# Kernel optimization log

Measured on AMD Instinct MI355X. Metric: run time of the kernel, lower is better.

## Reference

```python
import jax, jax.numpy as jnp
import numpy as np

T = 4096          # number of combine applications (segment length)
TRACE = 64        # trace_size (memory_size)
CTX = 64          # context_size


def setup_inputs() -> dict:
    key = jax.random.key(0)
    k1, k2, k3, k4 = jax.random.split(key, 4)
    shape = (T, TRACE, CTX)
    # deterministic FFM params (init_deterministic)
    a = jnp.linspace(1e-6, 0.5, TRACE).astype(jnp.float32)
    b = (2 * jnp.pi / jnp.linspace(1, 1000, CTX)).astype(jnp.float32)
    return {
        "a": a,
        "b": b,
        "state_re": jax.random.normal(k1, shape, jnp.float32),
        "state_im": jax.random.normal(k2, shape, jnp.float32),
        "x_re": jax.random.normal(k3, shape, jnp.float32),
        "x_im": jax.random.normal(k4, shape, jnp.float32),
        "i": jnp.ones((T,), jnp.int32),
        "j": jnp.ones((T,), jnp.int32),
    }


def reference(a, b, state_re, state_im, x_re, x_im, i, j):
    # log_gamma: (-|a| + i*b) * t, broadcast to [T, TRACE, CTX]
    t = j.astype(jnp.float32).reshape(-1, 1, 1)
    ab = jax.lax.complex(-jnp.abs(a).reshape(1, TRACE, 1),
                         b.reshape(1, 1, CTX))
    gamma = jnp.exp(ab * t)                       # complex decay/rotation gate
    state = jax.lax.complex(state_re, state_im)
    x = jax.lax.complex(x_re, x_im)
    new_state = state * gamma + x                 # binary associative combine
    return (jnp.real(new_state), jnp.imag(new_state), j + i)
```

## Files before the change

kernel.cpp:

```cpp
#include <hip/hip_runtime.h>


typedef float f32x4 __attribute__((ext_vector_type(4)));

constexpr int T_DIM  = 4096;
constexpr int N      = T_DIM * 64 * 64;
constexpr int N4     = N / 4;
constexpr int GRID   = 2048;
constexpr int BLOCK  = 256;
constexpr int STRIDE = GRID * BLOCK;
constexpr int TRIPS  = N4 / STRIDE;
constexpr int T_STEP = STRIDE >> 10;

__global__ __launch_bounds__(BLOCK, 8) void ffm_kernel(
    const float* __restrict__ a,
    const float* __restrict__ b,
    const float* __restrict__ s_re,
    const float* __restrict__ s_im,
    const float* __restrict__ x_re,
    const float* __restrict__ x_im,
    const int*   __restrict__ iv,
    const int*   __restrict__ jv,
    float* __restrict__ out)
{
    const int gtid = blockIdx.x * blockDim.x + threadIdx.x;

    if (gtid < T_DIM) {
        out[2 * N + gtid] = (float)(jv[gtid] + iv[gtid]);
    }

    const int c4 = (gtid & 15) << 2;
    const int m  = (gtid >> 4) & 63;
    const int t0 = gtid >> 10;

    const float am = fabsf(a[m]);
    const f32x4 bv = *reinterpret_cast<const f32x4*>(b + c4);

    int base = gtid << 2;

    f32x4 sr = *reinterpret_cast<const f32x4*>(s_re + base);
    f32x4 si = *reinterpret_cast<const f32x4*>(s_im + base);
    f32x4 xr = *reinterpret_cast<const f32x4*>(x_re + base);
    f32x4 xi = *reinterpret_cast<const f32x4*>(x_im + base);
    float tj = (float)jv[t0];

    #pragma unroll
    for (int trip = 0; trip < TRIPS; ++trip) {
        f32x4 nsr, nsi, nxr, nxi;
        float ntj = 0.f;
        const int nbase = base + (STRIDE << 2);
        if (trip + 1 < TRIPS) {
            nsr = *reinterpret_cast<const f32x4*>(s_re + nbase);
            nsi = *reinterpret_cast<const f32x4*>(s_im + nbase);
            nxr = *reinterpret_cast<const f32x4*>(x_re + nbase);
            nxi = *reinterpret_cast<const f32x4*>(x_im + nbase);
            ntj = (float)jv[t0 + (trip + 1) * T_STEP];
        }

        const float decay = __expf(-am * tj);
        f32x4 orv, oiv;
        #pragma unroll
        for (int k = 0; k < 4; ++k) {
            float s, c;
            __sincosf(bv[k] * tj, &s, &c);
            const float gre = decay * c;
            const float gim = decay * s;
            orv[k] = fmaf(sr[k], gre, fmaf(-si[k], gim, xr[k]));
            oiv[k] = fmaf(sr[k], gim, fmaf( si[k], gre, xi[k]));
        }

        *reinterpret_cast<f32x4*>(out + base)     = orv;
        *reinterpret_cast<f32x4*>(out + N + base) = oiv;

        if (trip + 1 < TRIPS) {
            sr = nsr; si = nsi; xr = nxr; xi = nxi; tj = ntj;
            base = nbase;
        }
    }
}

extern "C" void kernel_launch(void* const* d_in, const int* in_sizes, int n_in,
                              void* d_out, int out_size, void* d_ws, size_t ws_size,
                              hipStream_t stream) {
    const float* a    = (const float*)d_in[0];
    const float* b    = (const float*)d_in[1];
    const float* s_re = (const float*)d_in[2];
    const float* s_im = (const float*)d_in[3];
    const float* x_re = (const float*)d_in[4];
    const float* x_im = (const float*)d_in[5];
    const int*   iv   = (const int*)d_in[6];
    const int*   jv   = (const int*)d_in[7];
    float* out = (float*)d_out;

    ffm_kernel<<<GRID, BLOCK, 0, stream>>>(a, b, s_re, s_im, x_re, x_im, iv, jv, out);
}
```

Baseline: 81.10 us.

## Issue all loads up front per thread and double grid size

New measurement: 89.26 us. +10.1%, slower.

```diff
diff --git a/kernel.cpp b/kernel.cpp
--- a/kernel.cpp
+++ b/kernel.cpp
@@ -6,13 +6,12 @@
 constexpr int T_DIM  = 4096;
 constexpr int N      = T_DIM * 64 * 64;
 constexpr int N4     = N / 4;
-constexpr int GRID   = 2048;
+constexpr int GRID   = 4096;
 constexpr int BLOCK  = 256;
 constexpr int STRIDE = GRID * BLOCK;
-constexpr int TRIPS  = N4 / STRIDE;
-constexpr int T_STEP = STRIDE >> 10;
+constexpr int ITEMS  = N4 / STRIDE;
 
-__global__ __launch_bounds__(BLOCK, 8) void ffm_kernel(
+__global__ __launch_bounds__(BLOCK) void ffm_kernel(
     const float* __restrict__ a,
     const float* __restrict__ b,
     const float* __restrict__ s_re,
@@ -36,46 +35,40 @@
     const float am = fabsf(a[m]);
     const f32x4 bv = *reinterpret_cast<const f32x4*>(b + c4);
 
-    int base = gtid << 2;
+    float tj[ITEMS];
+    #pragma unroll
+    for (int i = 0; i < ITEMS; ++i) {
+        tj[i] = (float)jv[t0 + (i << 10)];
+    }
 
-    f32x4 sr = *reinterpret_cast<const f32x4*>(s_re + base);
-    f32x4 si = *reinterpret_cast<const f32x4*>(s_im + base);
-    f32x4 xr = *reinterpret_cast<const f32x4*>(x_re + base);
-    f32x4 xi = *reinterpret_cast<const f32x4*>(x_im + base);
-    float tj = (float)jv[t0];
+    f32x4 sr[ITEMS], si[ITEMS], xr[ITEMS], xi[ITEMS];
+    #pragma unroll
+    for (int i = 0; i < ITEMS; ++i) {
+        const int base = (gtid + i * STRIDE) << 2;
+        sr[i] = *reinterpret_cast<const f32x4*>(s_re + base);
+        si[i] = *reinterpret_cast<const f32x4*>(s_im + base);
+        xr[i] = *reinterpret_cast<const f32x4*>(x_re + base);
+        xi[i] = *reinterpret_cast<const f32x4*>(x_im + base);
+    }
+
+    __builtin_amdgcn_sched_barrier(0);
 
     #pragma unroll
-    for (int trip = 0; trip < TRIPS; ++trip) {
-        f32x4 nsr, nsi, nxr, nxi;
-        float ntj = 0.f;
-        const int nbase = base + (STRIDE << 2);
-        if (trip + 1 < TRIPS) {
-            nsr = *reinterpret_cast<const f32x4*>(s_re + nbase);
-            nsi = *reinterpret_cast<const f32x4*>(s_im + nbase);
-            nxr = *reinterpret_cast<const f32x4*>(x_re + nbase);
-            nxi = *reinterpret_cast<const f32x4*>(x_im + nbase);
-            ntj = (float)jv[t0 + (trip + 1) * T_STEP];
-        }
-
-        const float decay = __expf(-am * tj);
+    for (int i = 0; i < ITEMS; ++i) {
+        const float decay = __expf(-am * tj[i]);
         f32x4 orv, oiv;
         #pragma unroll
         for (int k = 0; k < 4; ++k) {
             float s, c;
-            __sincosf(bv[k] * tj, &s, &c);
+            __sincosf(bv[k] * tj[i], &s, &c);
             const float gre = decay * c;
             const float gim = decay * s;
-            orv[k] = fmaf(sr[k], gre, fmaf(-si[k], gim, xr[k]));
-            oiv[k] = fmaf(sr[k], gim, fmaf( si[k], gre, xi[k]));
+            orv[k] = fmaf(sr[i][k], gre, fmaf(-si[i][k], gim, xr[i][k]));
+            oiv[k] = fmaf(sr[i][k], gim, fmaf( si[i][k], gre, xi[i][k]));
         }
-
+        const int base = (gtid + i * STRIDE) << 2;
         *reinterpret_cast<f32x4*>(out + base)     = orv;
         *reinterpret_cast<f32x4*>(out + N + base) = oiv;
-
-        if (trip + 1 < TRIPS) {
-            sr = nsr; si = nsi; xr = nxr; xi = nxi; tj = ntj;
-            base = nbase;
-        }
     }
 }
 
```
